# Optimization experiments

Hardware: AMD Instinct MI355X
Metric: run time of the kernel (lower is better)

## Reference

```python
import jax, jax.numpy as jnp
import numpy as np

CODEBOOK_SIZE = 1024
LATENT_DIM = 64
BETA = 0.25
DECAY = 0.99
EPS = 1e-05


def _hadamard(n):
    H = np.array([[1.0]], dtype=np.float32)
    while H.shape[0] < n:
        H = np.kron(H, np.array([[1.0, 1.0], [1.0, -1.0]], dtype=np.float32))
    return H


def setup_inputs() -> dict:
    key = jax.random.key(0)
    k1, k2, k3 = jax.random.split(key, 3)
    x = jax.random.normal(k1, (16, LATENT_DIM, 64, 64), dtype=jnp.float32)
    lim = 1.0 / CODEBOOK_SIZE
    embedding_weight = jax.random.uniform(k2, (CODEBOOK_SIZE, LATENT_DIM), jnp.float32, -lim, lim)
    ema_w = jax.random.uniform(k3, (CODEBOOK_SIZE, LATENT_DIM), jnp.float32, -lim, lim)
    ema_cluster_size = jnp.ones((CODEBOOK_SIZE,), jnp.float32)
    rotation_matrix = jnp.asarray(_hadamard(LATENT_DIM))
    return {"x": x, "embedding_weight": embedding_weight, "rotation_matrix": rotation_matrix,
            "ema_cluster_size": ema_cluster_size, "ema_w": ema_w}


def reference(x, embedding_weight, rotation_matrix, ema_cluster_size, ema_w):
    sg = jax.lax.stop_gradient
    B, C, H, W = x.shape
    K, D = embedding_weight.shape
    # [B,C,H,W] -> [N, D]
    x_flat = jnp.transpose(x, (0, 2, 3, 1)).reshape(-1, D)
    x_rot = x_flat @ rotation_matrix
    # squared euclidean distances [N, K]
    dist = (jnp.sum(x_rot * x_rot, axis=-1, keepdims=True)
            + jnp.sum(embedding_weight * embedding_weight, axis=-1)[None, :]
            - 2.0 * (x_rot @ embedding_weight.T))
    idx = jnp.argmin(dist, axis=-1)  # [N]
    quant_flat = embedding_weight[idx]  # gather == one-hot @ E
    quant = jnp.transpose(quant_flat.reshape(B, H, W, C), (0, 3, 1, 2))
    commitment_loss = BETA * jnp.mean((sg(quant) - x) ** 2)
    codebook_loss = jnp.mean((quant - sg(x)) ** 2)
    N = x_flat.shape[0]
    counts = jax.ops.segment_sum(jnp.ones((N,), x.dtype), idx, num_segments=K)
    avg_probs = counts / N
    entropy_loss = -jnp.sum(avg_probs * jnp.log(avg_probs + 1e-10))
    loss = codebook_loss + commitment_loss + entropy_loss
    # EMA bookkeeping (training path; detached in the original)
    new_cs = ema_cluster_size * DECAY + (1.0 - DECAY) * counts
    n_tot = jnp.sum(new_cs)
    new_cs = (new_cs + EPS) / (n_tot + K * EPS) * n_tot
    dw = jax.ops.segment_sum(sg(x_rot), idx, num_segments=K)  # encodings.T @ x_rot
    new_ema_w = ema_w * DECAY + (1.0 - DECAY) * dw
    new_embedding = new_ema_w / new_cs[:, None]
    # straight-through estimator
    quant_out = x + sg(quant - x)
    return quant_out, loss, idx, new_embedding, new_cs, new_ema_w
```

## Files before the change

### kernel.cpp

```cpp
#include <hip/hip_runtime.h>
#include <cmath>

#define PAD 68


__global__ __launch_bounds__(256) void vq_init_kernel(const float* __restrict__ E,
                                                      float* __restrict__ ws) {
    #pragma clang fp contract(off)
    int g = blockIdx.x * 256 + threadIdx.x;
    ws[2048 + g] = 0.0f;
    if (g < 1024) {
        ws[1024 + g] = 0.0f;
        const float* e = E + g * 64;
        float r[8];
        #pragma unroll
        for (int j = 0; j < 8; ++j) r[j] = e[j] * e[j];
        #pragma unroll
        for (int t = 1; t < 8; ++t)
            #pragma unroll
            for (int j = 0; j < 8; ++j) {
                float sq = e[8 * t + j] * e[8 * t + j];
                r[j] = r[j] + sq;
            }
        ws[g] = ((r[0] + r[1]) + (r[2] + r[3])) + ((r[4] + r[5]) + (r[6] + r[7]));
    }
    if (g == 0) ws[67584] = 0.0f;
}

__global__ __launch_bounds__(256) void vq_main_kernel(
    const float* __restrict__ x, const float* __restrict__ E,
    const float* __restrict__ R, float* __restrict__ ws, float* __restrict__ out)
{
    #pragma clang fp contract(off)
    __shared__ float s_x[64][PAD];
    __shared__ float s_e[64][PAD];
    __shared__ float s_xr[64][PAD];
    __shared__ float s_ee[64];
    __shared__ float s_xx[64];
    __shared__ int   s_idx[64];
    __shared__ float s_red[8];

    const int tid = threadIdx.x;
    const int tc = tid >> 4;
    const int tr = tid & 15;
    const int brow = blockIdx.x;
    const int b = brow >> 6, h = brow & 63;

    const float* ee_g  = ws;
    float* counts  = ws + 1024;
    float* dw      = ws + 2048;
    float* mse_acc = ws + 67584;
    float* out_q   = out;
    float* out_idx = out + 4194305;

    const size_t xbase = (size_t)b * 262144 + (size_t)h * 64;

    #pragma unroll
    for (int i = 0; i < 4; ++i) {
        int d  = i * 16 + (tid >> 4);
        int w4 = (tid & 15) * 4;
        float4 v = *(const float4*)(x + xbase + (size_t)d * 4096 + w4);
        *(float4*)&s_x[d][w4] = v;
        float4 r = *(const float4*)(R + d * 64 + w4);
        *(float4*)&s_e[d][w4] = r;
    }
    __syncthreads();

    {
        float acc[4][4] = {};
        for (int d = 0; d < 64; ++d) {
            float xv[4], rv[4];
            #pragma unroll
            for (int i = 0; i < 4; ++i) xv[i] = s_x[d][tc + 16 * i];
            #pragma unroll
            for (int j = 0; j < 4; ++j) rv[j] = s_e[d][tr + 16 * j];
            #pragma unroll
            for (int i = 0; i < 4; ++i)
                #pragma unroll
                for (int j = 0; j < 4; ++j)
                    acc[i][j] = fmaf(xv[i], rv[j], acc[i][j]);
        }
        #pragma unroll
        for (int i = 0; i < 4; ++i)
            #pragma unroll
            for (int j = 0; j < 4; ++j)
                s_xr[tc + 16 * i][tr + 16 * j] = acc[i][j];
    }
    __syncthreads();

    if (tid < 64) {
        const int w = tid;
        float r[8];
        #pragma unroll
        for (int j = 0; j < 8; ++j) { float u = s_xr[w][j]; r[j] = u * u; }
        #pragma unroll
        for (int t = 1; t < 8; ++t)
            #pragma unroll
            for (int j = 0; j < 8; ++j) {
                float u = s_xr[w][8 * t + j];
                float sq = u * u;
                r[j] = r[j] + sq;
            }
        s_xx[w] = ((r[0] + r[1]) + (r[2] + r[3])) + ((r[4] + r[5]) + (r[6] + r[7]));
    }
    __syncthreads();

    float xxw[4];
    #pragma unroll
    for (int i = 0; i < 4; ++i) xxw[i] = s_xx[tc + 16 * i];

    float bestv[4]; int besti[4];
    #pragma unroll
    for (int i = 0; i < 4; ++i) { bestv[i] = 3.402823466e38f; besti[i] = 0; }

    for (int ch = 0; ch < 16; ++ch) {
        const int c0 = ch * 64;
        #pragma unroll
        for (int i = 0; i < 4; ++i) {
            int f = i * 256 + tid;
            int c = f >> 4, d4 = (f & 15) * 4;
            float4 v = *(const float4*)(E + (size_t)(c0 + c) * 64 + d4);
            *(float4*)&s_e[c][d4] = v;
        }
        if (tid < 64) s_ee[tid] = ee_g[c0 + tid];
        __syncthreads();

        float acc[4][4] = {};
        #pragma unroll
        for (int dq = 0; dq < 16; ++dq) {
            float4 xv[4], ev[4];
            #pragma unroll
            for (int i = 0; i < 4; ++i) xv[i] = *(const float4*)&s_xr[tc + 16 * i][dq * 4];
            #pragma unroll
            for (int j = 0; j < 4; ++j) ev[j] = *(const float4*)&s_e[tr + 16 * j][dq * 4];
            #pragma unroll
            for (int i = 0; i < 4; ++i)
                #pragma unroll
                for (int j = 0; j < 4; ++j) {
                    acc[i][j] = fmaf(xv[i].x, ev[j].x, acc[i][j]);
                    acc[i][j] = fmaf(xv[i].y, ev[j].y, acc[i][j]);
                    acc[i][j] = fmaf(xv[i].z, ev[j].z, acc[i][j]);
                    acc[i][j] = fmaf(xv[i].w, ev[j].w, acc[i][j]);
                }
        }
        #pragma unroll
        for (int j = 0; j < 4; ++j) {
            int c = c0 + tr + 16 * j;
            float eec = s_ee[tr + 16 * j];
            #pragma unroll
            for (int i = 0; i < 4; ++i) {
                float d1 = xxw[i] + eec;
                float m2 = 2.0f * acc[i][j];
                float dist = d1 - m2;
                if (dist < bestv[i]) { bestv[i] = dist; besti[i] = c; }
            }
        }
        __syncthreads();
    }

    #pragma unroll
    for (int i = 0; i < 4; ++i) {
        float v = bestv[i]; int ix = besti[i];
        #pragma unroll
        for (int m = 1; m < 16; m <<= 1) {
            float ov = __shfl_xor(v, m, 64);
            int   oi = __shfl_xor(ix, m, 64);
            if (ov < v || (ov == v && oi < ix)) { v = ov; ix = oi; }
        }
        const int w = tc + 16 * i;
        if (tr == 0) {
            s_idx[w] = ix;
            out_idx[brow * 64 + w] = (float)ix;
            unsafeAtomicAdd(&counts[ix], 1.0f);
        }
        float4 xr = *(const float4*)&s_xr[w][tr * 4];
        float* dst = dw + (size_t)ix * 64 + tr * 4;
        unsafeAtomicAdd(dst + 0, xr.x);
        unsafeAtomicAdd(dst + 1, xr.y);
        unsafeAtomicAdd(dst + 2, xr.z);
        unsafeAtomicAdd(dst + 3, xr.w);
    }
    __syncthreads();

    {
        int w = tid >> 2, p = (tid & 3) * 16;
        int ix = s_idx[w];
        const float* erow = E + (size_t)ix * 64 + p;
        float4 a  = *(const float4*)(erow + 0);
        float4 b4 = *(const float4*)(erow + 4);
        float4 c4 = *(const float4*)(erow + 8);
        float4 d4 = *(const float4*)(erow + 12);
        *(float4*)&s_e[w][p + 0]  = a;
        *(float4*)&s_e[w][p + 4]  = b4;
        *(float4*)&s_e[w][p + 8]  = c4;
        *(float4*)&s_e[w][p + 12] = d4;
    }
    __syncthreads();

    float mse = 0.0f;
    #pragma unroll
    for (int i = 0; i < 4; ++i) {
        int d  = i * 16 + (tid >> 4);
        int w4 = (tid & 15) * 4;
        float4 xv = *(const float4*)&s_x[d][w4];
        float q0 = s_e[w4 + 0][d], q1 = s_e[w4 + 1][d];
        float q2 = s_e[w4 + 2][d], q3 = s_e[w4 + 3][d];
        float4 o;
        o.x = xv.x + (q0 - xv.x);
        o.y = xv.y + (q1 - xv.y);
        o.z = xv.z + (q2 - xv.z);
        o.w = xv.w + (q3 - xv.w);
        float dx = q0 - xv.x, dy = q1 - xv.y, dz = q2 - xv.z, dv = q3 - xv.w;
        mse = fmaf(dx, dx, mse); mse = fmaf(dy, dy, mse);
        mse = fmaf(dz, dz, mse); mse = fmaf(dv, dv, mse);
        *(float4*)(out_q + xbase + (size_t)d * 4096 + w4) = o;
    }
    #pragma unroll
    for (int off = 32; off > 0; off >>= 1) mse += __shfl_down(mse, off, 64);
    int wave = tid >> 6, lane = tid & 63;
    if (lane == 0) s_red[wave] = mse;
    __syncthreads();
    if (tid == 0)
        unsafeAtomicAdd(mse_acc, s_red[0] + s_red[1] + s_red[2] + s_red[3]);
}

__global__ __launch_bounds__(1024) void vq_finalize_kernel(
    const float* __restrict__ ema_cs, const float* __restrict__ ema_w,
    const float* __restrict__ ws, float* __restrict__ out)
{
    __shared__ float s_ncs[1024];
    __shared__ float s_red[32];
    const int t = threadIdx.x;
    const float* counts = ws + 1024;
    const float* dw     = ws + 2048;
    const float  mse    = ws[67584];

    float cnt = counts[t];
    float p   = cnt * (1.0f / 65536.0f);
    float ent = -p * logf(p + 1e-10f);
    float ncs = ema_cs[t] * 0.99f + 0.01f * cnt;

    float a = ncs, e2 = ent;
    #pragma unroll
    for (int off = 32; off > 0; off >>= 1) {
        a  += __shfl_down(a,  off, 64);
        e2 += __shfl_down(e2, off, 64);
    }
    const int wave = t >> 6;
    if ((t & 63) == 0) { s_red[wave] = a; s_red[16 + wave] = e2; }
    __syncthreads();
    if (t == 0) {
        float sa = 0.0f, se = 0.0f;
        for (int i = 0; i < 16; ++i) { sa += s_red[i]; se += s_red[16 + i]; }
        s_red[0] = sa; s_red[16] = se;
    }
    __syncthreads();
    const float n_tot = s_red[0], ent_tot = s_red[16];

    float ncs_s = (ncs + 1e-5f) / (n_tot + 1024.0f * 1e-5f) * n_tot;
    s_ncs[t] = ncs_s;

    float* out_loss = out + 4194304;
    float* out_emb  = out + 4259841;
    float* out_cs   = out + 4325377;
    float* out_emaw = out + 4326401;

    out_cs[t] = ncs_s;
    if (t == 0) out_loss[0] = 1.25f * (mse * (1.0f / 4194304.0f)) + ent_tot;
    __syncthreads();

    for (int i = 0; i < 64; ++i) {
        int e = i * 1024 + t;
        float nw = ema_w[e] * 0.99f + 0.01f * dw[e];
        out_emaw[e] = nw;
        out_emb[e]  = nw / s_ncs[e >> 6];
    }
}

extern "C" void kernel_launch(void* const* d_in, const int* in_sizes, int n_in,
                              void* d_out, int out_size, void* d_ws, size_t ws_size,
                              hipStream_t stream) {
    const float* x      = (const float*)d_in[0];
    const float* E      = (const float*)d_in[1];
    const float* R      = (const float*)d_in[2];
    const float* ema_cs = (const float*)d_in[3];
    const float* ema_w  = (const float*)d_in[4];
    float* out = (float*)d_out;
    float* ws  = (float*)d_ws;

    hipLaunchKernelGGL(vq_init_kernel,     dim3(256),  dim3(256),  0, stream, E, ws);
    hipLaunchKernelGGL(vq_main_kernel,     dim3(1024), dim3(256),  0, stream, x, E, R, ws, out);
    hipLaunchKernelGGL(vq_finalize_kernel, dim3(1),    dim3(1024), 0, stream, ema_cs, ema_w, ws, out);
}
```

Baseline: 267.1 us.

## Cut main kernel shared memory and parallelize EMA finalize across blocks

```diff
diff --git a/kernel.cpp b/kernel.cpp
--- a/kernel.cpp
+++ b/kernel.cpp
@@ -27,14 +27,13 @@
     if (g == 0) ws[67584] = 0.0f;
 }
 
-__global__ __launch_bounds__(256) void vq_main_kernel(
+__global__ __launch_bounds__(256, 4) void vq_main_kernel(
     const float* __restrict__ x, const float* __restrict__ E,
     const float* __restrict__ R, float* __restrict__ ws, float* __restrict__ out)
 {
     #pragma clang fp contract(off)
-    __shared__ float s_x[64][PAD];
-    __shared__ float s_e[64][PAD];
-    __shared__ float s_xr[64][PAD];
+    __shared__ float s_A[64][PAD];
+    __shared__ float s_B[64][PAD];
     __shared__ float s_ee[64];
     __shared__ float s_xx[64];
     __shared__ int   s_idx[64];
@@ -60,9 +59,9 @@
         int d  = i * 16 + (tid >> 4);
         int w4 = (tid & 15) * 4;
         float4 v = *(const float4*)(x + xbase + (size_t)d * 4096 + w4);
-        *(float4*)&s_x[d][w4] = v;
+        *(float4*)&s_A[d][w4] = v;
         float4 r = *(const float4*)(R + d * 64 + w4);
-        *(float4*)&s_e[d][w4] = r;
+        *(float4*)&s_B[d][w4] = r;
     }
     __syncthreads();
 
@@ -71,20 +70,21 @@
         for (int d = 0; d < 64; ++d) {
             float xv[4], rv[4];
             #pragma unroll
-            for (int i = 0; i < 4; ++i) xv[i] = s_x[d][tc + 16 * i];
-            #pragma unroll
-            for (int j = 0; j < 4; ++j) rv[j] = s_e[d][tr + 16 * j];
+            for (int i = 0; i < 4; ++i) xv[i] = s_A[d][tc + 16 * i];
+            #pragma unroll
+            for (int j = 0; j < 4; ++j) rv[j] = s_B[d][tr + 16 * j];
             #pragma unroll
             for (int i = 0; i < 4; ++i)
                 #pragma unroll
                 for (int j = 0; j < 4; ++j)
                     acc[i][j] = fmaf(xv[i], rv[j], acc[i][j]);
         }
+        __syncthreads();
         #pragma unroll
         for (int i = 0; i < 4; ++i)
             #pragma unroll
             for (int j = 0; j < 4; ++j)
-                s_xr[tc + 16 * i][tr + 16 * j] = acc[i][j];
+                s_B[tc + 16 * i][tr + 16 * j] = acc[i][j];
     }
     __syncthreads();
 
@@ -92,12 +92,12 @@
         const int w = tid;
         float r[8];
         #pragma unroll
-        for (int j = 0; j < 8; ++j) { float u = s_xr[w][j]; r[j] = u * u; }
+        for (int j = 0; j < 8; ++j) { float u = s_B[w][j]; r[j] = u * u; }
         #pragma unroll
         for (int t = 1; t < 8; ++t)
             #pragma unroll
             for (int j = 0; j < 8; ++j) {
-                float u = s_xr[w][8 * t + j];
+                float u = s_B[w][8 * t + j];
                 float sq = u * u;
                 r[j] = r[j] + sq;
             }
@@ -120,7 +120,7 @@
             int f = i * 256 + tid;
             int c = f >> 4, d4 = (f & 15) * 4;
             float4 v = *(const float4*)(E + (size_t)(c0 + c) * 64 + d4);
-            *(float4*)&s_e[c][d4] = v;
+            *(float4*)&s_A[c][d4] = v;
         }
         if (tid < 64) s_ee[tid] = ee_g[c0 + tid];
         __syncthreads();
@@ -130,18 +130,29 @@
         for (int dq = 0; dq < 16; ++dq) {
             float4 xv[4], ev[4];
             #pragma unroll
-            for (int i = 0; i < 4; ++i) xv[i] = *(const float4*)&s_xr[tc + 16 * i][dq * 4];
-            #pragma unroll
-            for (int j = 0; j < 4; ++j) ev[j] = *(const float4*)&s_e[tr + 16 * j][dq * 4];
-            #pragma unroll
-            for (int i = 0; i < 4; ++i)
-                #pragma unroll
-                for (int j = 0; j < 4; ++j) {
+            for (int i = 0; i < 4; ++i) xv[i] = *(const float4*)&s_B[tc + 16 * i][dq * 4];
+            #pragma unroll
+            for (int j = 0; j < 4; ++j) ev[j] = *(const float4*)&s_A[tr + 16 * j][dq * 4];
+            #pragma unroll
+            for (int i = 0; i < 4; ++i)
+                #pragma unroll
+                for (int j = 0; j < 4; ++j)
                     acc[i][j] = fmaf(xv[i].x, ev[j].x, acc[i][j]);
+            #pragma unroll
+            for (int i = 0; i < 4; ++i)
+                #pragma unroll
+                for (int j = 0; j < 4; ++j)
                     acc[i][j] = fmaf(xv[i].y, ev[j].y, acc[i][j]);
+            #pragma unroll
+            for (int i = 0; i < 4; ++i)
+                #pragma unroll
+                for (int j = 0; j < 4; ++j)
                     acc[i][j] = fmaf(xv[i].z, ev[j].z, acc[i][j]);
+            #pragma unroll
+            for (int i = 0; i < 4; ++i)
+                #pragma unroll
+                for (int j = 0; j < 4; ++j)
                     acc[i][j] = fmaf(xv[i].w, ev[j].w, acc[i][j]);
-                }
         }
         #pragma unroll
         for (int j = 0; j < 4; ++j) {
@@ -173,7 +184,7 @@
             out_idx[brow * 64 + w] = (float)ix;
             unsafeAtomicAdd(&counts[ix], 1.0f);
         }
-        float4 xr = *(const float4*)&s_xr[w][tr * 4];
+        float4 xr = *(const float4*)&s_B[w][tr * 4];
         float* dst = dw + (size_t)ix * 64 + tr * 4;
         unsafeAtomicAdd(dst + 0, xr.x);
         unsafeAtomicAdd(dst + 1, xr.y);
@@ -190,10 +201,10 @@
         float4 b4 = *(const float4*)(erow + 4);
         float4 c4 = *(const float4*)(erow + 8);
         float4 d4 = *(const float4*)(erow + 12);
-        *(float4*)&s_e[w][p + 0]  = a;
-        *(float4*)&s_e[w][p + 4]  = b4;
-        *(float4*)&s_e[w][p + 8]  = c4;
-        *(float4*)&s_e[w][p + 12] = d4;
+        *(float4*)&s_A[w][p + 0]  = a;
+        *(float4*)&s_A[w][p + 4]  = b4;
+        *(float4*)&s_A[w][p + 8]  = c4;
+        *(float4*)&s_A[w][p + 12] = d4;
     }
     __syncthreads();
 
@@ -202,9 +213,9 @@
     for (int i = 0; i < 4; ++i) {
         int d  = i * 16 + (tid >> 4);
         int w4 = (tid & 15) * 4;
-        float4 xv = *(const float4*)&s_x[d][w4];
-        float q0 = s_e[w4 + 0][d], q1 = s_e[w4 + 1][d];
-        float q2 = s_e[w4 + 2][d], q3 = s_e[w4 + 3][d];
+        float4 xv = *(const float4*)(x + xbase + (size_t)d * 4096 + w4);
+        float q0 = s_A[w4 + 0][d], q1 = s_A[w4 + 1][d];
+        float q2 = s_A[w4 + 2][d], q3 = s_A[w4 + 3][d];
         float4 o;
         o.x = xv.x + (q0 - xv.x);
         o.y = xv.y + (q1 - xv.y);
@@ -224,15 +235,12 @@
         unsafeAtomicAdd(mse_acc, s_red[0] + s_red[1] + s_red[2] + s_red[3]);
 }
 
-__global__ __launch_bounds__(1024) void vq_finalize_kernel(
-    const float* __restrict__ ema_cs, const float* __restrict__ ema_w,
-    const float* __restrict__ ws, float* __restrict__ out)
+__global__ __launch_bounds__(1024) void vq_reduce_kernel(
+    const float* __restrict__ ema_cs, float* __restrict__ ws, float* __restrict__ out)
 {
-    __shared__ float s_ncs[1024];
     __shared__ float s_red[32];
     const int t = threadIdx.x;
     const float* counts = ws + 1024;
-    const float* dw     = ws + 2048;
     const float  mse    = ws[67584];
 
     float cnt = counts[t];
@@ -258,22 +266,43 @@
     const float n_tot = s_red[0], ent_tot = s_red[16];
 
     float ncs_s = (ncs + 1e-5f) / (n_tot + 1024.0f * 1e-5f) * n_tot;
-    s_ncs[t] = ncs_s;
-
-    float* out_loss = out + 4194304;
+    out[4325377 + t] = ncs_s;
+    if (t == 0) {
+        out[4194304] = 1.25f * (mse * (1.0f / 4194304.0f)) + ent_tot;
+        ws[67585] = n_tot;
+    }
+}
+
+__global__ __launch_bounds__(256) void vq_update_kernel(
+    const float* __restrict__ ema_cs, const float* __restrict__ ema_w,
+    const float* __restrict__ ws, float* __restrict__ out)
+{
+    __shared__ float s_inv[64];
+    const int t = threadIdx.x;
+    const int base_code = blockIdx.x * 64;
+    const float* counts = ws + 1024;
+    const float* dw     = ws + 2048;
+    const float  n_tot  = ws[67585];
+
+    if (t < 64) {
+        int code = base_code + t;
+        float ncs = ema_cs[code] * 0.99f + 0.01f * counts[code];
+        float ncs_s = (ncs + 1e-5f) / (n_tot + 1024.0f * 1e-5f) * n_tot;
+        s_inv[t] = 1.0f / ncs_s;
+    }
+    __syncthreads();
+
     float* out_emb  = out + 4259841;
-    float* out_cs   = out + 4325377;
     float* out_emaw = out + 4326401;
-
-    out_cs[t] = ncs_s;
-    if (t == 0) out_loss[0] = 1.25f * (mse * (1.0f / 4194304.0f)) + ent_tot;
-    __syncthreads();
-
-    for (int i = 0; i < 64; ++i) {
-        int e = i * 1024 + t;
+    const int base_e = base_code * 64;
+
+    #pragma unroll
+    for (int k = 0; k < 16; ++k) {
+        int el = k * 256 + t;
+        int e  = base_e + el;
         float nw = ema_w[e] * 0.99f + 0.01f * dw[e];
         out_emaw[e] = nw;
-        out_emb[e]  = nw / s_ncs[e >> 6];
+        out_emb[e]  = nw * s_inv[el >> 6];
     }
 }
 
@@ -288,7 +317,8 @@
     float* out = (float*)d_out;
     float* ws  = (float*)d_ws;
 
-    hipLaunchKernelGGL(vq_init_kernel,     dim3(256),  dim3(256),  0, stream, E, ws);
-    hipLaunchKernelGGL(vq_main_kernel,     dim3(1024), dim3(256),  0, stream, x, E, R, ws, out);
-    hipLaunchKernelGGL(vq_finalize_kernel, dim3(1),    dim3(1024), 0, stream, ema_cs, ema_w, ws, out);
-}
+    hipLaunchKernelGGL(vq_init_kernel,   dim3(256),  dim3(256),  0, stream, E, ws);
+    hipLaunchKernelGGL(vq_main_kernel,   dim3(1024), dim3(256),  0, stream, x, E, R, ws, out);
+    hipLaunchKernelGGL(vq_reduce_kernel, dim3(1),    dim3(1024), 0, stream, ema_cs, ws, out);
+    hipLaunchKernelGGL(vq_update_kernel, dim3(16),   dim3(256),  0, stream, ema_cs, ema_w, ws, out);
+}
```

Result: faster. 251.9 us (-5.7%).
